# Performance work log

Hardware: AMD Instinct MI355X
Metric: run time of the kernel (lower is better)

The kernel has to match this reference:

```python
import jax, jax.numpy as jnp
import numpy as np

OBS_DIM = 83
HIDDEN = 128
INTENT = 64
HEADS = 4
HEAD_DIM = INTENT // HEADS  # 16
BATCH = 16384
NNBR = 32


def setup_inputs() -> dict:
    key = jax.random.key(0)
    ks = jax.random.split(key, 12)
    s = 0.05
    return {
        "self_obs": jax.random.normal(ks[0], (BATCH, OBS_DIM), jnp.float32),
        "neighbor_obs": jax.random.normal(ks[1], (BATCH, NNBR, OBS_DIM), jnp.float32),
        "edge_weights": jax.random.uniform(ks[2], (BATCH, NNBR), jnp.float32),
        # IntentEncoder params: Linear(83,128) -> ReLU -> Linear(128,64) -> Tanh
        "W1": jax.random.normal(ks[3], (OBS_DIM, HIDDEN), jnp.float32) * s,
        "b1": jnp.zeros((HIDDEN,), jnp.float32),
        "W2": jax.random.normal(ks[4], (HIDDEN, INTENT), jnp.float32) * s,
        "b2": jnp.zeros((INTENT,), jnp.float32),
        # GAT params
        "Wa": jax.random.normal(ks[5], (2 * INTENT, 1), jnp.float32) * s,
        "ba": jnp.zeros((1,), jnp.float32),
        "Wv": jax.random.normal(ks[6], (INTENT, HEADS * HEAD_DIM), jnp.float32) * s,
        "bv": jnp.zeros((HEADS * HEAD_DIM,), jnp.float32),
        "Wo": jax.random.normal(ks[7], (HEADS * HEAD_DIM, HEAD_DIM), jnp.float32) * s,
        "bo": jnp.zeros((HEAD_DIM,), jnp.float32),
    }


def _encode(x, W1, b1, W2, b2):
    h = jax.nn.relu(x @ W1 + b1)
    return jnp.tanh(h @ W2 + b2)


def reference(self_obs, neighbor_obs, edge_weights, W1, b1, W2, b2, Wa, ba, Wv, bv, Wo, bo):
    B, N = neighbor_obs.shape[:2]
    self_intent = _encode(self_obs, W1, b1, W2, b2)              # (B, 64)
    nbr_intent = _encode(neighbor_obs, W1, b1, W2, b2)           # (B, N, 64)
    # attention logits: leaky_relu(Linear(concat[self, nbr]))
    self_exp = jnp.broadcast_to(self_intent[:, None, :], (B, N, INTENT))
    concat = jnp.concatenate([self_exp, nbr_intent], axis=-1)    # (B, N, 128)
    e = jax.nn.leaky_relu(concat @ Wa + ba, negative_slope=0.2)  # (B, N, 1)
    e = e * edge_weights[..., None]
    alpha = jax.nn.softmax(e, axis=1)                            # (B, N, 1)
    values = (nbr_intent @ Wv + bv).reshape(B, N, HEADS, HEAD_DIM)
    agg = jnp.sum(alpha[:, :, None, :] * values, axis=1)         # (B, H, D)
    agg = agg.reshape(B, HEADS * HEAD_DIM)
    return agg @ Wo + bo                                         # (B, 16)
```

## Files before the change

### kernel.cpp

```cpp
#include <hip/hip_runtime.h>


typedef _Float16 half8 __attribute__((ext_vector_type(8)));
typedef __fp16 fp16x2 __attribute__((ext_vector_type(2)));
typedef __fp16 fp16x8 __attribute__((ext_vector_type(8)));
typedef float f32x4 __attribute__((ext_vector_type(4)));

struct __attribute__((packed, aligned(4))) F4 { f32x4 v; };

__device__ __forceinline__ f32x4 ld4(const float* p) {
    return ((const F4*)p)->v;
}

#define MFMA16(a, b, c) __builtin_amdgcn_mfma_f32_16x16x32_f16((a), (b), (c), 0, 0, 0)

#define WS_W1F   0
#define WS_W2F   24576
#define WS_WVOF  40960
#define WS_WAFN  45056
#define WS_BVO   49152
#define WS_STAGE 49216
#define WS_WASF  49216
#define WS_ES    53312

__device__ __forceinline__ half8 pack8(float a0, float a1, float a2, float a3,
                                       float a4, float a5, float a6, float a7) {
    fp16x2 p0 = __builtin_amdgcn_cvt_pkrtz(a0, a1);
    fp16x2 p1 = __builtin_amdgcn_cvt_pkrtz(a2, a3);
    fp16x2 p2 = __builtin_amdgcn_cvt_pkrtz(a4, a5);
    fp16x2 p3 = __builtin_amdgcn_cvt_pkrtz(a6, a7);
    fp16x8 h;
    h[0] = p0[0]; h[1] = p0[1]; h[2] = p1[0]; h[3] = p1[1];
    h[4] = p2[0]; h[5] = p2[1]; h[6] = p3[0]; h[7] = p3[1];
    return __builtin_bit_cast(half8, h);
}

__global__ void prep_kernel(const float* __restrict__ W1, const float* __restrict__ b1,
                            const float* __restrict__ W2, const float* __restrict__ Wv,
                            const float* __restrict__ Wa, const float* __restrict__ Wo,
                            const float* __restrict__ bv, const float* __restrict__ bo,
                            char* __restrict__ ws) {
    int t = blockIdx.x * 256 + threadIdx.x;
    _Float16* W1f = (_Float16*)(ws + WS_W1F);
    _Float16* W2f = (_Float16*)(ws + WS_W2F);
    float* Wvof = (float*)(ws + WS_WVOF);
    float* Wafn = (float*)(ws + WS_WAFN);
    float* Wasf = (float*)(ws + WS_WASF);
    float* bvo  = (float*)(ws + WS_BVO);

    if (t < 12288) {
        int i = t & 7, lane = (t >> 3) & 63, rest = t >> 9;
        int kt = rest % 3, hm = rest / 3;
        int g = lane >> 4, m = lane & 15;
        int k = 32 * kt + 8 * g + i, h = 16 * hm + m;
        float v = (k < 83) ? W1[k * 128 + h] : (k == 83 ? b1[h] : 0.f);
        W1f[t] = (_Float16)v;
    } else if (t < 20480) {
        int u = t - 12288;
        int i = u & 7, lane = (u >> 3) & 63, rest = u >> 9;
        int kt = rest & 3, om = rest >> 2;
        int g = lane >> 4, m = lane & 15;
        int h = 16 * (2 * kt + (i >> 2)) + 4 * g + (i & 3);
        W2f[u] = (_Float16)W2[h * 64 + 16 * om + m];
    } else if (t < 21504) {
        int u = t - 20480; int lane = u >> 4, idx = u & 15;
        int g = lane >> 4, m = lane & 15;
        int o = 16 * (idx >> 2) + 4 * g + (idx & 3);
        float acc = 0.f;
#pragma unroll 8
        for (int k = 0; k < 64; ++k) acc += Wv[o * 64 + k] * Wo[k * 16 + m];
        Wvof[u] = acc;
    } else if (t < 22528) {
        int u = t - 21504; int lane = u >> 4, idx = u & 15;
        int g = lane >> 4;
        int o = 16 * (idx >> 2) + 4 * g + (idx & 3);
        Wafn[u] = Wa[64 + o];
    } else if (t < 23552) {
        int u = t - 22528; int lane = u >> 4, idx = u & 15;
        int g = lane >> 4;
        int o = 16 * (idx >> 2) + 4 * g + (idx & 3);
        Wasf[u] = Wa[o];
    } else if (t < 23568) {
        int u = t - 23552;
        float s = bo[u];
#pragma unroll 8
        for (int k = 0; k < 64; ++k) s += bv[k] * Wo[k * 16 + u];
        bvo[u] = s;
    }
}

__device__ __forceinline__ void load_raw(const float* __restrict__ src,
                                         int g, int m, f32x4 raw[2][6]) {
#pragma unroll
    for (int rn = 0; rn < 2; ++rn) {
        const float* rp = src + (16 * rn + m) * 83;
        raw[rn][0] = ld4(rp + 8 * g);
        raw[rn][1] = ld4(rp + 8 * g + 4);
        raw[rn][2] = ld4(rp + 32 + 8 * g);
        raw[rn][3] = ld4(rp + 32 + 8 * g + 4);
        const float* p2 = (g < 2) ? (rp + 64 + 8 * g) : (g == 2 ? rp + 79 : rp);
        raw[rn][4] = ld4(p2);
        raw[rn][5] = ld4((g < 2) ? p2 + 4 : p2);
    }
}

__device__ __forceinline__ void pack_xf(const f32x4 raw[2][6], int g,
                                        half8 xf[2][3]) {
    const half8 hz = {0, 0, 0, 0, 0, 0, 0, 0};
#pragma unroll
    for (int rn = 0; rn < 2; ++rn) {
        xf[rn][0] = pack8(raw[rn][0][0], raw[rn][0][1], raw[rn][0][2], raw[rn][0][3],
                          raw[rn][1][0], raw[rn][1][1], raw[rn][1][2], raw[rn][1][3]);
        xf[rn][1] = pack8(raw[rn][2][0], raw[rn][2][1], raw[rn][2][2], raw[rn][2][3],
                          raw[rn][3][0], raw[rn][3][1], raw[rn][3][2], raw[rn][3][3]);
        half8 h;
        if (g < 2) {
            h = pack8(raw[rn][4][0], raw[rn][4][1], raw[rn][4][2], raw[rn][4][3],
                      raw[rn][5][0], raw[rn][5][1], raw[rn][5][2], raw[rn][5][3]);
        } else if (g == 2) {
            h = pack8(raw[rn][4][1], raw[rn][4][2], raw[rn][4][3], 1.f,
                      0.f, 0.f, 0.f, 0.f);
        } else {
            h = hz;
        }
        xf[rn][2] = h;
    }
}

__device__ __forceinline__ void mlp_from_xf(const half8 xf[2][3],
                                            const char* wlds,
                                            const float* __restrict__ b2,
                                            int lane, int g, float I[4][2][4]) {
    const half8* W1f = (const half8*)(wlds + WS_W1F);
    const half8* W2f = (const half8*)(wlds + WS_W2F);
    const f32x4 zz = {0.f, 0.f, 0.f, 0.f};

    half8 hf[4][2];
#pragma unroll
    for (int t = 0; t < 4; ++t) {
        int h0 = 2 * t, h1 = 2 * t + 1;
        half8 u0 = W1f[(h0 * 3 + 0) * 64 + lane];
        half8 u1 = W1f[(h0 * 3 + 1) * 64 + lane];
        half8 u2 = W1f[(h0 * 3 + 2) * 64 + lane];
        half8 v0 = W1f[(h1 * 3 + 0) * 64 + lane];
        half8 v1 = W1f[(h1 * 3 + 1) * 64 + lane];
        half8 v2 = W1f[(h1 * 3 + 2) * 64 + lane];
#pragma unroll
        for (int rn = 0; rn < 2; ++rn) {
            f32x4 a = zz, b = zz;
            a = MFMA16(u0, xf[rn][0], a);
            a = MFMA16(u1, xf[rn][1], a);
            a = MFMA16(u2, xf[rn][2], a);
            b = MFMA16(v0, xf[rn][0], b);
            b = MFMA16(v1, xf[rn][1], b);
            b = MFMA16(v2, xf[rn][2], b);
            hf[t][rn] = pack8(
                fmaxf(a[0], 0.f), fmaxf(a[1], 0.f), fmaxf(a[2], 0.f), fmaxf(a[3], 0.f),
                fmaxf(b[0], 0.f), fmaxf(b[1], 0.f), fmaxf(b[2], 0.f), fmaxf(b[3], 0.f));
        }
    }

#pragma unroll
    for (int om = 0; om < 4; ++om) {
        half8 w0 = W2f[(om * 4 + 0) * 64 + lane];
        half8 w1 = W2f[(om * 4 + 1) * 64 + lane];
        half8 w2 = W2f[(om * 4 + 2) * 64 + lane];
        half8 w3 = W2f[(om * 4 + 3) * 64 + lane];
        float b2v[4];
#pragma unroll
        for (int r = 0; r < 4; ++r) b2v[r] = b2[16 * om + 4 * g + r];
#pragma unroll
        for (int rn = 0; rn < 2; ++rn) {
            f32x4 a = zz;
            a = MFMA16(w0, hf[0][rn], a);
            a = MFMA16(w1, hf[1][rn], a);
            a = MFMA16(w2, hf[2][rn], a);
            a = MFMA16(w3, hf[3][rn], a);
#pragma unroll
            for (int r = 0; r < 4; ++r) {
                float y = a[r] + b2v[r];
                float e = __expf(2.f * y);
                I[om][rn][r] = fmaf(-2.f, __builtin_amdgcn_rcpf(e + 1.f), 1.f);
            }
        }
    }
}

__global__ void __launch_bounds__(512, 3)
self_kernel(const float* __restrict__ sobs,
            const float* __restrict__ b2,
            char* __restrict__ ws) {
    __shared__ __align__(16) char wlds[40960];
    int tid = threadIdx.x, w = tid >> 6, lane = tid & 63;
    int g = lane >> 4, m = lane & 15;
    int r0 = (blockIdx.x * 8 + w) * 32;

    f32x4 raw[2][6];
    load_raw(sobs + (size_t)r0 * 83, g, m, raw);

    {
        const f32x4* s4 = (const f32x4*)ws;
        f32x4* d4 = (f32x4*)wlds;
#pragma unroll
        for (int t = 0; t < 5; ++t) d4[t * 512 + tid] = s4[t * 512 + tid];
        __syncthreads();
    }

    half8 xf[2][3];
    pack_xf(raw, g, xf);
    float I[4][2][4];
    mlp_from_xf(xf, wlds, b2, lane, g, I);

    const float* Wasf = (const float*)(ws + WS_WASF);
    float* es = (float*)(ws + WS_ES);

    float was[16];
#pragma unroll
    for (int idx = 0; idx < 16; ++idx) was[idx] = Wasf[lane * 16 + idx];

    float d0 = 0.f, d1 = 0.f;
#pragma unroll
    for (int om = 0; om < 4; ++om)
#pragma unroll
        for (int r = 0; r < 4; ++r) {
            d0 = fmaf(I[om][0][r], was[om * 4 + r], d0);
            d1 = fmaf(I[om][1][r], was[om * 4 + r], d1);
        }
    d0 += __shfl_xor(d0, 16); d0 += __shfl_xor(d0, 32);
    d1 += __shfl_xor(d1, 16); d1 += __shfl_xor(d1, 32);

    if (lane < 16) {
        es[r0 + lane] = d0;
        es[r0 + 16 + lane] = d1;
    }
}

__global__ void __launch_bounds__(512, 3)
main_kernel(const float* __restrict__ nbr,
            const float* __restrict__ edgew,
            const float* __restrict__ b2,
            const float* __restrict__ ba,
            const char* __restrict__ ws,
            float* __restrict__ out) {
    __shared__ __align__(16) char wlds[WS_STAGE];
    int tid = threadIdx.x, w = tid >> 6, lane = tid & 63;
    int b = blockIdx.x * 8 + w;
    int g = lane >> 4, m = lane & 15;

    f32x4 raw[2][6];
    load_raw(nbr + (size_t)b * 2656, g, m, raw);
    const float* es = (const float*)(ws + WS_ES);
    float esb = es[b];
    float ew0 = edgew[b * 32 + m];
    float ew1 = edgew[b * 32 + 16 + m];
    float bav = ba[0];

    {
        const f32x4* s4 = (const f32x4*)ws;
        f32x4* d4 = (f32x4*)wlds;
#pragma unroll
        for (int t = 0; t < 6; ++t) d4[t * 512 + tid] = s4[t * 512 + tid];
        if (tid < 4) d4[3072 + tid] = s4[3072 + tid];
        __syncthreads();
    }

    half8 xf[2][3];
    pack_xf(raw, g, xf);
    float I[4][2][4];
    mlp_from_xf(xf, wlds, b2, lane, g, I);

    const float* Wafn = (const float*)(wlds + WS_WAFN);
    const float* Wvof = (const float*)(wlds + WS_WVOF);
    const float* bvo  = (const float*)(wlds + WS_BVO);

    float en0 = 0.f, en1 = 0.f;
#pragma unroll
    for (int om = 0; om < 4; ++om)
#pragma unroll
        for (int r = 0; r < 4; ++r) {
            float wa = Wafn[lane * 16 + om * 4 + r];
            en0 = fmaf(I[om][0][r], wa, en0);
            en1 = fmaf(I[om][1][r], wa, en1);
        }
    en0 += __shfl_xor(en0, 16); en0 += __shfl_xor(en0, 32);
    en1 += __shfl_xor(en1, 16); en1 += __shfl_xor(en1, 32);

    float e0 = esb + en0 + bav; e0 = (e0 > 0.f) ? e0 : 0.2f * e0; e0 *= ew0;
    float e1 = esb + en1 + bav; e1 = (e1 > 0.f) ? e1 : 0.2f * e1; e1 *= ew1;

    float p0 = __expf(e0), p1 = __expf(e1);
    float s = p0 + p1;
#pragma unroll
    for (int msk = 1; msk <= 8; msk <<= 1) s += __shfl_xor(s, msk);
    float inv = __builtin_amdgcn_rcpf(s);
    float a0 = p0 * inv, a1 = p1 * inv;

    float wi[16];
#pragma unroll
    for (int om = 0; om < 4; ++om)
#pragma unroll
        for (int r = 0; r < 4; ++r)
            wi[om * 4 + r] = a0 * I[om][0][r] + a1 * I[om][1][r];
#pragma unroll
    for (int idx = 0; idx < 16; ++idx) {
#pragma unroll
        for (int msk = 1; msk <= 8; msk <<= 1)
            wi[idx] += __shfl_xor(wi[idx], msk);
    }

    float val = 0.f;
#pragma unroll
    for (int idx = 0; idx < 16; ++idx)
        val = fmaf(wi[idx], Wvof[lane * 16 + idx], val);
    val += __shfl_xor(val, 16);
    val += __shfl_xor(val, 32);

    if (lane < 16) out[(size_t)b * 16 + lane] = val + bvo[lane];
}

extern "C" void kernel_launch(void* const* d_in, const int* in_sizes, int n_in,
                              void* d_out, int out_size, void* d_ws, size_t ws_size,
                              hipStream_t stream) {
    const float* self_obs = (const float*)d_in[0];
    const float* nbr      = (const float*)d_in[1];
    const float* ew       = (const float*)d_in[2];
    const float* W1       = (const float*)d_in[3];
    const float* b1       = (const float*)d_in[4];
    const float* W2       = (const float*)d_in[5];
    const float* b2       = (const float*)d_in[6];
    const float* Wa       = (const float*)d_in[7];
    const float* ba       = (const float*)d_in[8];
    const float* Wv       = (const float*)d_in[9];
    const float* bv       = (const float*)d_in[10];
    const float* Wo       = (const float*)d_in[11];
    const float* bo       = (const float*)d_in[12];
    char* ws = (char*)d_ws;
    float* out = (float*)d_out;

    prep_kernel<<<93, 256, 0, stream>>>(W1, b1, W2, Wv, Wa, Wo, bv, bo, ws);
    self_kernel<<<64, 512, 0, stream>>>(self_obs, b2, ws);
    main_kernel<<<2048, 512, 0, stream>>>(nbr, ew, b2, ba, ws, out);
}
```

Before: 58.66 us.

## Compute value projection with MFMA on fp16 Wvo and vectorize attention weights

Replaces the per-lane 16-element weighted-sum reduction (64 cross-lane shuffles) and scalar Wvo dot product with fp16 MFMA calls that project each neighbor's intent through the fused Wv·Wo matrix. Attention weights are applied afterwards, which leaves only 4 values per lane to reduce. The fused Wv·Wo weight is stored in fp16 in a fragment layout, which shrinks the workspace and the LDS staging copy. The Wa neighbor weights are relaid so each lane reads one float4. Lower precision in the value projection adds rounding error.

```diff
diff --git a/kernel.cpp b/kernel.cpp
--- a/kernel.cpp
+++ b/kernel.cpp
@@ -14,14 +14,14 @@
 
 #define MFMA16(a, b, c) __builtin_amdgcn_mfma_f32_16x16x32_f16((a), (b), (c), 0, 0, 0)
 
-#define WS_W1F   0
-#define WS_W2F   24576
-#define WS_WVOF  40960
-#define WS_WAFN  45056
-#define WS_BVO   49152
-#define WS_STAGE 49216
-#define WS_WASF  49216
-#define WS_ES    53312
+#define WS_W1F    0
+#define WS_W2F    24576
+#define WS_WVO16  40960
+#define WS_WAFN   43008
+#define WS_BVO    47104
+#define WS_STAGE  47168
+#define WS_WASF   47168
+#define WS_ES     51264
 
 __device__ __forceinline__ half8 pack8(float a0, float a1, float a2, float a3,
                                        float a4, float a5, float a6, float a7) {
@@ -43,7 +43,7 @@
     int t = blockIdx.x * 256 + threadIdx.x;
     _Float16* W1f = (_Float16*)(ws + WS_W1F);
     _Float16* W2f = (_Float16*)(ws + WS_W2F);
-    float* Wvof = (float*)(ws + WS_WVOF);
+    _Float16* Wvo16 = (_Float16*)(ws + WS_WVO16);
     float* Wafn = (float*)(ws + WS_WAFN);
     float* Wasf = (float*)(ws + WS_WASF);
     float* bvo  = (float*)(ws + WS_BVO);
@@ -63,18 +63,19 @@
         int h = 16 * (2 * kt + (i >> 2)) + 4 * g + (i & 3);
         W2f[u] = (_Float16)W2[h * 64 + 16 * om + m];
     } else if (t < 21504) {
-        int u = t - 20480; int lane = u >> 4, idx = u & 15;
+        int u = t - 20480;
+        int i = u & 7, lane = (u >> 3) & 63, kt = u >> 9;
         int g = lane >> 4, m = lane & 15;
-        int o = 16 * (idx >> 2) + 4 * g + (idx & 3);
+        int o = 16 * (2 * kt + (i >> 2)) + 4 * g + (i & 3);
         float acc = 0.f;
 #pragma unroll 8
         for (int k = 0; k < 64; ++k) acc += Wv[o * 64 + k] * Wo[k * 16 + m];
-        Wvof[u] = acc;
+        Wvo16[u] = (_Float16)acc;
     } else if (t < 22528) {
-        int u = t - 21504; int lane = u >> 4, idx = u & 15;
+        int u = t - 21504;
+        int c = u & 3, lane = (u >> 2) & 63, om = u >> 8;
         int g = lane >> 4;
-        int o = 16 * (idx >> 2) + 4 * g + (idx & 3);
-        Wafn[u] = Wa[64 + o];
+        Wafn[u] = Wa[64 + 16 * om + 4 * g + c];
     } else if (t < 23552) {
         int u = t - 22528; int lane = u >> 4, idx = u & 15;
         int g = lane >> 4;
@@ -246,6 +247,7 @@
     int tid = threadIdx.x, w = tid >> 6, lane = tid & 63;
     int b = blockIdx.x * 8 + w;
     int g = lane >> 4, m = lane & 15;
+    const f32x4 zz = {0.f, 0.f, 0.f, 0.f};
 
     f32x4 raw[2][6];
     load_raw(nbr + (size_t)b * 2656, g, m, raw);
@@ -259,8 +261,8 @@
         const f32x4* s4 = (const f32x4*)ws;
         f32x4* d4 = (f32x4*)wlds;
 #pragma unroll
-        for (int t = 0; t < 6; ++t) d4[t * 512 + tid] = s4[t * 512 + tid];
-        if (tid < 4) d4[3072 + tid] = s4[3072 + tid];
+        for (int t = 0; t < 5; ++t) d4[t * 512 + tid] = s4[t * 512 + tid];
+        if (tid < 388) d4[2560 + tid] = s4[2560 + tid];
         __syncthreads();
     }
 
@@ -269,19 +271,20 @@
     float I[4][2][4];
     mlp_from_xf(xf, wlds, b2, lane, g, I);
 
-    const float* Wafn = (const float*)(wlds + WS_WAFN);
-    const float* Wvof = (const float*)(wlds + WS_WVOF);
-    const float* bvo  = (const float*)(wlds + WS_BVO);
+    const f32x4* Wafn2 = (const f32x4*)(wlds + WS_WAFN);
+    const half8* Wvo16 = (const half8*)(wlds + WS_WVO16);
+    const float* bvo   = (const float*)(wlds + WS_BVO);
 
     float en0 = 0.f, en1 = 0.f;
 #pragma unroll
-    for (int om = 0; om < 4; ++om)
+    for (int om = 0; om < 4; ++om) {
+        f32x4 wa = Wafn2[om * 64 + lane];
 #pragma unroll
         for (int r = 0; r < 4; ++r) {
-            float wa = Wafn[lane * 16 + om * 4 + r];
-            en0 = fmaf(I[om][0][r], wa, en0);
-            en1 = fmaf(I[om][1][r], wa, en1);
-        }
+            en0 = fmaf(I[om][0][r], wa[r], en0);
+            en1 = fmaf(I[om][1][r], wa[r], en1);
+        }
+    }
     en0 += __shfl_xor(en0, 16); en0 += __shfl_xor(en0, 32);
     en1 += __shfl_xor(en1, 16); en1 += __shfl_xor(en1, 32);
 
@@ -295,27 +298,37 @@
     float inv = __builtin_amdgcn_rcpf(s);
     float a0 = p0 * inv, a1 = p1 * inv;
 
-    float wi[16];
-#pragma unroll
-    for (int om = 0; om < 4; ++om)
-#pragma unroll
-        for (int r = 0; r < 4; ++r)
-            wi[om * 4 + r] = a0 * I[om][0][r] + a1 * I[om][1][r];
-#pragma unroll
-    for (int idx = 0; idx < 16; ++idx) {
-#pragma unroll
-        for (int msk = 1; msk <= 8; msk <<= 1)
-            wi[idx] += __shfl_xor(wi[idx], msk);
-    }
-
-    float val = 0.f;
-#pragma unroll
-    for (int idx = 0; idx < 16; ++idx)
-        val = fmaf(wi[idx], Wvof[lane * 16 + idx], val);
-    val += __shfl_xor(val, 16);
-    val += __shfl_xor(val, 32);
-
-    if (lane < 16) out[(size_t)b * 16 + lane] = val + bvo[lane];
+    half8 vf[2][2];
+#pragma unroll
+    for (int kt = 0; kt < 2; ++kt)
+#pragma unroll
+        for (int rn = 0; rn < 2; ++rn)
+            vf[kt][rn] = pack8(I[2 * kt][rn][0], I[2 * kt][rn][1],
+                               I[2 * kt][rn][2], I[2 * kt][rn][3],
+                               I[2 * kt + 1][rn][0], I[2 * kt + 1][rn][1],
+                               I[2 * kt + 1][rn][2], I[2 * kt + 1][rn][3]);
+
+    half8 wv0 = Wvo16[lane];
+    half8 wv1 = Wvo16[64 + lane];
+    f32x4 acc0 = zz, acc1 = zz;
+    acc0 = MFMA16(wv0, vf[0][0], acc0);
+    acc0 = MFMA16(wv1, vf[1][0], acc0);
+    acc1 = MFMA16(wv0, vf[0][1], acc1);
+    acc1 = MFMA16(wv1, vf[1][1], acc1);
+
+    f32x4 v4;
+#pragma unroll
+    for (int r = 0; r < 4; ++r) v4[r] = a0 * acc0[r] + a1 * acc1[r];
+#pragma unroll
+    for (int msk = 1; msk <= 8; msk <<= 1) {
+#pragma unroll
+        for (int r = 0; r < 4; ++r) v4[r] += __shfl_xor(v4[r], msk);
+    }
+
+    if (m == 0) {
+        f32x4 bb = *(const f32x4*)(bvo + 4 * g);
+        *(f32x4*)(out + (size_t)b * 16 + 4 * g) = v4 + bb;
+    }
 }
 
 extern "C" void kernel_launch(void* const* d_in, const int* in_sizes, int n_in,
```

New measurement: 58.42 us. About the same (-0.4%).
